# Kernel tuning notes

Measured on AMD Instinct MI355X. Metric: run time of the kernel, lower is better.

The kernel has to match this reference:

```python
import jax, jax.numpy as jnp
import numpy as np

B, S, V, F, H = 256, 512, 50000, 64, 256


def setup_inputs() -> dict:
    key = jax.random.key(0)
    ks = jax.random.split(key, 12)
    s_in = 1.0 / np.sqrt(F)
    s_hid = 1.0 / np.sqrt(H)
    return {
        "batch": jax.random.randint(ks[0], (B, S), 0, V),
        "features": jax.random.normal(ks[1], (V, F), jnp.float32),
        "W_ih0": jax.random.normal(ks[2], (H, F), jnp.float32) * s_in,
        "W_hh0": jax.random.normal(ks[3], (H, H), jnp.float32) * s_hid,
        "b_ih0": jax.random.normal(ks[4], (H,), jnp.float32) * s_hid,
        "b_hh0": jax.random.normal(ks[5], (H,), jnp.float32) * s_hid,
        "W_ih1": jax.random.normal(ks[6], (H, H), jnp.float32) * s_hid,
        "W_hh1": jax.random.normal(ks[7], (H, H), jnp.float32) * s_hid,
        "b_ih1": jax.random.normal(ks[8], (H,), jnp.float32) * s_hid,
        "b_hh1": jax.random.normal(ks[9], (H,), jnp.float32) * s_hid,
        "W_out": jax.random.normal(ks[10], (V, H), jnp.float32) * s_hid,
        "b_out": jax.random.normal(ks[11], (V,), jnp.float32) * s_hid,
    }


def _rnn_layer(x, W_ih, W_hh, b_ih, b_hh):
    # x: [B, S, Din] -> [B, S, H]; torch tanh RNN: h_t = tanh(x_t W_ih^T + b_ih + h_{t-1} W_hh^T + b_hh)
    xW = jnp.einsum('bsd,hd->bsh', x, W_ih) + (b_ih + b_hh)  # precompute input projection
    h0 = jnp.zeros((x.shape[0], W_hh.shape[0]), x.dtype)

    def step(h, xt):
        h = jnp.tanh(xt + h @ W_hh.T)
        return h, h

    _, ys = jax.lax.scan(step, h0, jnp.swapaxes(xW, 0, 1))  # scan over time
    return jnp.swapaxes(ys, 0, 1)


def reference(batch, features, W_ih0, W_hh0, b_ih0, b_hh0,
              W_ih1, W_hh1, b_ih1, b_hh1, W_out, b_out):
    # vectorized replacement of the nested per-token gather loop
    full_representation = features[batch]            # [B, S, F]
    h = _rnn_layer(full_representation, W_ih0, W_hh0, b_ih0, b_hh0)
    h = _rnn_layer(h, W_ih1, W_hh1, b_ih1, b_hh1)    # [B, S, H]
    return h[:, -1, :] @ W_out.T + b_out             # [B, V]
```

## Files before the change

### kernel.cpp

```cpp
#include <hip/hip_runtime.h>

#define B_ 256
#define S_ 512
#define V_ 50000
#define F_ 64
#define H_ 256

typedef _Float16 f16;
typedef _Float16 f16x2 __attribute__((ext_vector_type(2)));
typedef _Float16 f16x4 __attribute__((ext_vector_type(4)));
typedef _Float16 f16x8 __attribute__((ext_vector_type(8)));
typedef float f32x4 __attribute__((ext_vector_type(4)));

#define MFMA(a, b, c) __builtin_amdgcn_mfma_f32_16x16x32_f16((a), (b), (c), 0, 0, 0)

__device__ __forceinline__ f16x8 cvt8(const float4 a, const float4 b) {
    f16x8 v;
    v[0] = (f16)a.x; v[1] = (f16)a.y; v[2] = (f16)a.z; v[3] = (f16)a.w;
    v[4] = (f16)b.x; v[5] = (f16)b.y; v[6] = (f16)b.z; v[7] = (f16)b.w;
    return v;
}

__device__ __forceinline__ float fast_tanh(float x) {
    float e = __expf(2.f * x);
    float r = __builtin_amdgcn_rcpf(e + 1.f);
    return __builtin_fmaf(-2.f, r, 1.f);
}

__device__ __forceinline__ f32x4 cvt4f(const f16x4 v) {
    f32x4 r; r[0] = (float)v[0]; r[1] = (float)v[1]; r[2] = (float)v[2]; r[3] = (float)v[3];
    return r;
}
__device__ __forceinline__ f16x4 pack4(const f32x4 a, const f32x4 b) {
    f16x4 r; r[0] = (f16)(a[0] + b[0]); r[1] = (f16)(a[1] + b[1]);
    r[2] = (f16)(a[2] + b[2]); r[3] = (f16)(a[3] + b[3]);
    return r;
}
__device__ __forceinline__ f16x4 tanh4(const f32x4 a, const f32x4 b) {
    f16x4 r;
#pragma unroll
    for (int i = 0; i < 4; ++i) r[i] = (f16)fast_tanh(a[i] + b[i]);
    return r;
}

__global__ void k_init_flags(int* flags) {
    if (threadIdx.x < 128) flags[threadIdx.x] = 0;
}

__global__ __launch_bounds__(512) void k_vocab_proj(
    const float* __restrict__ feat, const float* __restrict__ Wih,
    const float* __restrict__ bi, const float* __restrict__ bh,
    f16* __restrict__ T)
{
    __shared__ char Wl[256 * 128];
    __shared__ char Xl[16 * 128];
    const int tid = threadIdx.x;
    {
        const int n = tid >> 1, k0 = (tid & 1) << 5;
#pragma unroll
        for (int k = k0; k < k0 + 32; k += 8) {
            float4 a = *(const float4*)(Wih + n * F_ + k);
            float4 b = *(const float4*)(Wih + n * F_ + k + 4);
            *(f16x8*)(Wl + n * 128 + (((k >> 3) ^ (n & 7)) << 4)) = cvt8(a, b);
        }
    }
    const int v0 = blockIdx.x * 16;
    {
        const int m = tid >> 5, k = (tid & 31) << 1;
        float2 a = *(const float2*)(feat + (v0 + m) * F_ + k);
        f16x2 v; v[0] = (f16)a.x; v[1] = (f16)a.y;
        *(f16x2*)(Xl + m * 128 + ((((k >> 3) ^ (m & 7)) << 4) | ((k & 7) << 1))) = v;
    }
    __syncthreads();
    const int lane = tid & 63, w = tid >> 6;
    const int q = lane & 15, g = lane >> 4;
#pragma unroll
    for (int nt = 0; nt < 2; ++nt) {
        const int n0 = w * 32 + nt * 16;
        const int nrow = n0 + q;
        float4 b1 = *(const float4*)(bi + n0 + g * 4);
        float4 b2 = *(const float4*)(bh + n0 + g * 4);
        f32x4 acc = {b1.x + b2.x, b1.y + b2.y, b1.z + b2.z, b1.w + b2.w};
#pragma unroll
        for (int kb = 0; kb < 2; ++kb) {
            f16x8 a = *(const f16x8*)(Wl + nrow * 128 + (((kb * 4 + g) ^ (nrow & 7)) << 4));
            f16x8 b = *(const f16x8*)(Xl + q * 128 + (((kb * 4 + g) ^ (q & 7)) << 4));
            acc = MFMA(a, b, acc);
        }
        f16x4 o; o[0] = (f16)acc[0]; o[1] = (f16)acc[1]; o[2] = (f16)acc[2]; o[3] = (f16)acc[3];
        *(f16x4*)(T + (size_t)(v0 + q) * H_ + n0 + g * 4) = o;
    }
}

__global__ __launch_bounds__(512) __attribute__((amdgpu_waves_per_eu(2, 2)))
void k_rnn_split(
    const f16* __restrict__ T, const int* __restrict__ idx,
    const float* __restrict__ Whh0, const float* __restrict__ Wih1,
    const float* __restrict__ bih1, const float* __restrict__ bhh1,
    const float* __restrict__ Whh1,
    f16* __restrict__ pbuf, int* flags, f16* __restrict__ h1out)
{
    __shared__ char hb[2][8192];
    const int wg = blockIdx.x;
    const int tid = threadIdx.x, lane = tid & 63, w = tid >> 6;
    const int q = lane & 15, g = lane >> 4;
    const int ncol = w * 32;
    const int swz = (q & 7) << 4;

    int rbase[2], wbase[2];
#pragma unroll
    for (int p2 = 0; p2 < 2; ++p2)
        rbase[p2] = q * 512 + ((p2 * 64 + g * 16) ^ swz);
#pragma unroll
    for (int tt = 0; tt < 2; ++tt)
        wbase[tt] = q * 512 + (((ncol + tt * 16 + g * 4) * 2) ^ swz);

    const int pr = (wg < 16) ? wg : wg - 16;
    const int brow = pr * 16 + q;
    const size_t prow = (size_t)brow * 512;

#define FRD(kb_, RD_) (*(const f16x8*)(hb[RD_] + rbase[(kb_) & 1] + (((kb_) >> 1) * 128)))
#define HWR(tt_, WR_) (*(f16x4*)(hb[WR_] + wbase[tt_]))
#define STEP_BAR() do { \
        asm volatile("s_waitcnt lgkmcnt(0)" ::: "memory"); \
        __builtin_amdgcn_s_barrier(); \
    } while (0)

    if (wg < 16) {
        f16x8 wA[2][8], wP[2][8];
#pragma unroll
        for (int tt = 0; tt < 2; ++tt) {
            const int n = ncol + tt * 16 + q;
#pragma unroll
            for (int kb = 0; kb < 8; ++kb) {
                const int o = n * H_ + kb * 32 + g * 8;
                wA[tt][kb] = cvt8(*(const float4*)(Whh0 + o), *(const float4*)(Whh0 + o + 4));
                wP[tt][kb] = cvt8(*(const float4*)(Wih1 + o), *(const float4*)(Wih1 + o + 4));
            }
        }
        f32x4 bs1[2];
#pragma unroll
        for (int tt = 0; tt < 2; ++tt) {
            const int n = ncol + tt * 16 + g * 4;
            float4 x = *(const float4*)(bih1 + n);
            float4 y = *(const float4*)(bhh1 + n);
            bs1[tt][0] = x.x + y.x; bs1[tt][1] = x.y + y.y;
            bs1[tt][2] = x.z + y.z; bs1[tt][3] = x.w + y.w;
        }
        {
            f32x4 z = {0.f, 0.f, 0.f, 0.f};
            *(f32x4*)(hb[1] + tid * 16) = z;
        }
        const int* idxr = idx + brow * S_;
        int* myflag = flags + wg * 8 + w;
        f16x4 xa[2], xb[2];
        {
            const size_t r0 = (size_t)idxr[0] * H_, r1 = (size_t)idxr[1] * H_;
#pragma unroll
            for (int tt = 0; tt < 2; ++tt) {
                xa[tt] = *(const f16x4*)(T + r0 + ncol + tt * 16 + g * 4);
                xb[tt] = *(const f16x4*)(T + r1 + ncol + tt * 16 + g * 4);
            }
        }
        int iA = idxr[2], iB = idxr[3];
        __syncthreads();

#define PBODY(XV, ID, RD, WR, T_) do {                                          \
                \
        f16x8 bf0 = FRD(0, RD), bf1 = FRD(1, RD), bf2 = FRD(2, RD),             \
              bf3 = FRD(3, RD), bf4 = FRD(4, RD), bf5 = FRD(5, RD),             \
              bf6 = FRD(6, RD), bf7 = FRD(7, RD);                               \
        f32x4 aL[2], aH[2];                                                     \
        _Pragma("unroll")                                                       \
        for (int tt = 0; tt < 2; ++tt) {                                        \
            aL[tt] = cvt4f(XV[tt]);                                             \
            aH[tt][0] = 0.f; aH[tt][1] = 0.f; aH[tt][2] = 0.f; aH[tt][3] = 0.f; \
        }                                                                       \
        {                 \
            const size_t rr = (size_t)ID * H_;                                  \
            _Pragma("unroll")                                                   \
            for (int tt = 0; tt < 2; ++tt)                                      \
                XV[tt] = *(const f16x4*)(T + rr + ncol + tt * 16 + g * 4);      \
            const int t4 = ((T_) + 4 < S_) ? (T_) + 4 : S_ - 1;                 \
            ID = idxr[t4];                                                      \
        }                                                                       \
                                               \
        _Pragma("unroll")                                                       \
        for (int tt = 0; tt < 2; ++tt) {                                        \
            aL[tt] = MFMA(wA[tt][0], bf0, aL[tt]);                              \
            aH[tt] = MFMA(wA[tt][4], bf4, aH[tt]);                              \
            aL[tt] = MFMA(wA[tt][1], bf1, aL[tt]);                              \
            aH[tt] = MFMA(wA[tt][5], bf5, aH[tt]);                              \
            aL[tt] = MFMA(wA[tt][2], bf2, aL[tt]);                              \
            aH[tt] = MFMA(wA[tt][6], bf6, aH[tt]);                              \
            aL[tt] = MFMA(wA[tt][3], bf3, aL[tt]);                              \
            aH[tt] = MFMA(wA[tt][7], bf7, aH[tt]);                              \
        }                                                                       \
                                  \
        _Pragma("unroll")                                                       \
        for (int tt = 0; tt < 2; ++tt) HWR(tt, WR) = tanh4(aL[tt], aH[tt]);     \
                  \
        f32x4 pL[2], pH[2];                                                     \
        _Pragma("unroll")                                                       \
        for (int tt = 0; tt < 2; ++tt) {                                        \
            pL[tt] = bs1[tt];                                                   \
            pH[tt][0] = 0.f; pH[tt][1] = 0.f; pH[tt][2] = 0.f; pH[tt][3] = 0.f; \
            pL[tt] = MFMA(wP[tt][0], bf0, pL[tt]);                              \
            pH[tt] = MFMA(wP[tt][4], bf4, pH[tt]);                              \
            pL[tt] = MFMA(wP[tt][1], bf1, pL[tt]);                              \
            pH[tt] = MFMA(wP[tt][5], bf5, pH[tt]);                              \
            pL[tt] = MFMA(wP[tt][2], bf2, pL[tt]);                              \
            pH[tt] = MFMA(wP[tt][6], bf6, pH[tt]);                              \
            pL[tt] = MFMA(wP[tt][3], bf3, pL[tt]);                              \
            pH[tt] = MFMA(wP[tt][7], bf7, pH[tt]);                              \
            *(f16x4*)(pbuf + (prow + (T_) - 1) * 256 + ncol + tt * 16 + g * 4)  \
                = pack4(pL[tt], pH[tt]);                                        \
        }                                                                       \
        if ((((T_) & 7) == 0) && lane == 0)                                     \
            __hip_atomic_store(myflag, (T_), __ATOMIC_RELEASE,                  \
                               __HIP_MEMORY_SCOPE_AGENT);                       \
        STEP_BAR();                                                             \
    } while (0)

        {
            f16x8 bf0 = FRD(0, 1), bf1 = FRD(1, 1), bf2 = FRD(2, 1), bf3 = FRD(3, 1),
                  bf4 = FRD(4, 1), bf5 = FRD(5, 1), bf6 = FRD(6, 1), bf7 = FRD(7, 1);
            f32x4 aL[2], aH[2];
#pragma unroll
            for (int tt = 0; tt < 2; ++tt) {
                aL[tt] = cvt4f(xa[tt]);
                aH[tt][0] = 0.f; aH[tt][1] = 0.f; aH[tt][2] = 0.f; aH[tt][3] = 0.f;
            }
            {
                const size_t rr = (size_t)iA * H_;
#pragma unroll
                for (int tt = 0; tt < 2; ++tt)
                    xa[tt] = *(const f16x4*)(T + rr + ncol + tt * 16 + g * 4);
                iA = idxr[4];
            }
#pragma unroll
            for (int tt = 0; tt < 2; ++tt) {
                aL[tt] = MFMA(wA[tt][0], bf0, aL[tt]);
                aH[tt] = MFMA(wA[tt][4], bf4, aH[tt]);
                aL[tt] = MFMA(wA[tt][1], bf1, aL[tt]);
                aH[tt] = MFMA(wA[tt][5], bf5, aH[tt]);
                aL[tt] = MFMA(wA[tt][2], bf2, aL[tt]);
                aH[tt] = MFMA(wA[tt][6], bf6, aH[tt]);
                aL[tt] = MFMA(wA[tt][3], bf3, aL[tt]);
                aH[tt] = MFMA(wA[tt][7], bf7, aH[tt]);
                HWR(tt, 0) = tanh4(aL[tt], aH[tt]);
            }
            STEP_BAR();
        }
        for (int t = 1; t < 511; t += 2) {
            PBODY(xb, iB, 0, 1, t);
            PBODY(xa, iA, 1, 0, t + 1);
        }
        PBODY(xb, iB, 0, 1, 511);
        {
            f16x8 bf0 = FRD(0, 1), bf1 = FRD(1, 1), bf2 = FRD(2, 1), bf3 = FRD(3, 1),
                  bf4 = FRD(4, 1), bf5 = FRD(5, 1), bf6 = FRD(6, 1), bf7 = FRD(7, 1);
            f32x4 pL[2], pH[2];
#pragma unroll
            for (int tt = 0; tt < 2; ++tt) {
                pL[tt] = bs1[tt];
                pH[tt][0] = 0.f; pH[tt][1] = 0.f; pH[tt][2] = 0.f; pH[tt][3] = 0.f;
                pL[tt] = MFMA(wP[tt][0], bf0, pL[tt]);
                pH[tt] = MFMA(wP[tt][4], bf4, pH[tt]);
                pL[tt] = MFMA(wP[tt][1], bf1, pL[tt]);
                pH[tt] = MFMA(wP[tt][5], bf5, pH[tt]);
                pL[tt] = MFMA(wP[tt][2], bf2, pL[tt]);
                pH[tt] = MFMA(wP[tt][6], bf6, pH[tt]);
                pL[tt] = MFMA(wP[tt][3], bf3, pL[tt]);
                pH[tt] = MFMA(wP[tt][7], bf7, pH[tt]);
                *(f16x4*)(pbuf + (prow + 511) * 256 + ncol + tt * 16 + g * 4)
                    = pack4(pL[tt], pH[tt]);
            }
        }
        if (lane == 0)
            __hip_atomic_store(myflag, 512, __ATOMIC_RELEASE, __HIP_MEMORY_SCOPE_AGENT);
#undef PBODY
    } else {
        f16x8 wC[2][8];
#pragma unroll
        for (int tt = 0; tt < 2; ++tt) {
            const int n = ncol + tt * 16 + q;
#pragma unroll
            for (int kb = 0; kb < 8; ++kb) {
                const int o = n * H_ + kb * 32 + g * 8;
                wC[tt][kb] = cvt8(*(const float4*)(Whh1 + o), *(const float4*)(Whh1 + o + 4));
            }
        }
        {   f32x4 z = {0.f, 0.f, 0.f, 0.f}; *(f32x4*)(hb[1] + tid * 16) = z; }
        const int* fl = flags + pr * 8;
        __syncthreads();

#define SPIN(need) do {                                                         \
        int mn;                                                                 \
        do {                                                                    \
            mn = 0x7fffffff;                                                    \
            _Pragma("unroll")                                                   \
            for (int i = 0; i < 8; ++i) {                                       \
                int v = __hip_atomic_load(fl + i, __ATOMIC_RELAXED,             \
                                          __HIP_MEMORY_SCOPE_AGENT);            \
                mn = v < mn ? v : mn;                                           \
            }                                                                   \
        } while (mn < (need));                                                  \
        __builtin_amdgcn_fence(__ATOMIC_ACQUIRE, "agent");                      \
    } while (0)

#define CBODY(PV, RD, WR, T_) do {                                              \
        f16x8 cf0 = FRD(0, RD), cf1 = FRD(1, RD), cf2 = FRD(2, RD),             \
              cf3 = FRD(3, RD), cf4 = FRD(4, RD), cf5 = FRD(5, RD),             \
              cf6 = FRD(6, RD), cf7 = FRD(7, RD);                               \
        f32x4 aL[2], aH[2];                                                     \
        _Pragma("unroll")                                                       \
        for (int tt = 0; tt < 2; ++tt) {                                        \
            aL[tt] = cvt4f(PV[tt]);                                             \
            aH[tt][0] = 0.f; aH[tt][1] = 0.f; aH[tt][2] = 0.f; aH[tt][3] = 0.f; \
        }                                                                       \
        {                                                                       \
            const int tr = ((T_) + 2 < S_) ? (T_) + 2 : S_ - 1;                 \
            _Pragma("unroll")                                                   \
            for (int tt = 0; tt < 2; ++tt)                                      \
                PV[tt] = *(const f16x4*)(pbuf + (prow + tr) * 256 + ncol + tt * 16 + g * 4); \
        }                                                                       \
        _Pragma("unroll")                                                       \
        for (int tt = 0; tt < 2; ++tt) {                                        \
            aL[tt] = MFMA(wC[tt][0], cf0, aL[tt]);                              \
            aH[tt] = MFMA(wC[tt][4], cf4, aH[tt]);                              \
            aL[tt] = MFMA(wC[tt][1], cf1, aL[tt]);                              \
            aH[tt] = MFMA(wC[tt][5], cf5, aH[tt]);                              \
            aL[tt] = MFMA(wC[tt][2], cf2, aL[tt]);                              \
            aH[tt] = MFMA(wC[tt][6], cf6, aH[tt]);                              \
            aL[tt] = MFMA(wC[tt][3], cf3, aL[tt]);                              \
            aH[tt] = MFMA(wC[tt][7], cf7, aH[tt]);                              \
        }                                                                       \
        _Pragma("unroll")                                                       \
        for (int tt = 0; tt < 2; ++tt) {                                        \
            f16x4 hv = tanh4(aL[tt], aH[tt]);                                   \
            HWR(tt, WR) = hv;                                                   \
            if ((T_) == S_ - 1)                                                 \
                *(f16x4*)(h1out + (size_t)brow * H_ + ncol + tt * 16 + g * 4) = hv; \
        }                                                                       \
        STEP_BAR();                                                             \
    } while (0)

        f16x4 pa[2], pb[2];
        SPIN(6);
#pragma unroll
        for (int tt = 0; tt < 2; ++tt) {
            pa[tt] = *(const f16x4*)(pbuf + (prow + 0) * 256 + ncol + tt * 16 + g * 4);
            pb[tt] = *(const f16x4*)(pbuf + (prow + 1) * 256 + ncol + tt * 16 + g * 4);
        }
        for (int tb = 0; tb < 512; tb += 4) {
            if (tb) {
                const int need = (tb + 6 < 512) ? tb + 6 : 512;
                SPIN(need);
            }
            CBODY(pa, 1, 0, tb);
            CBODY(pb, 0, 1, tb + 1);
            CBODY(pa, 1, 0, tb + 2);
            CBODY(pb, 0, 1, tb + 3);
        }
#undef CBODY
#undef SPIN
    }
#undef FRD
#undef HWR
#undef STEP_BAR
}

__global__ __launch_bounds__(512) void k_out(
    const f16* __restrict__ h1, const float* __restrict__ Wout,
    const float* __restrict__ bout, float* __restrict__ out)
{
    __shared__ char Hl[256 * 512];
    const int tid = threadIdx.x;
    {
        const int m = tid >> 1, half = tid & 1;
#pragma unroll
        for (int i = 0; i < 16; ++i) {
            const int blk = half * 16 + i;
            f16x8 v = *(const f16x8*)(h1 + m * H_ + blk * 8);
            *(f16x8*)(Hl + m * 512 + ((blk ^ (m & 7)) << 4)) = v;
        }
    }
    __syncthreads();
    const int lane = tid & 63, w = tid >> 6;
    const int q = lane & 15, g = lane >> 4;
    const int v0 = blockIdx.x * 80;
    f32x4 acc[5][2];
#pragma unroll
    for (int vt = 0; vt < 5; ++vt) {
        float4 bo = *(const float4*)(bout + v0 + vt * 16 + g * 4);
#pragma unroll
        for (int bt = 0; bt < 2; ++bt) {
            acc[vt][bt][0] = bo.x; acc[vt][bt][1] = bo.y;
            acc[vt][bt][2] = bo.z; acc[vt][bt][3] = bo.w;
        }
    }
#pragma unroll
    for (int kb = 0; kb < 8; ++kb) {
        f16x8 bf[2];
#pragma unroll
        for (int bt = 0; bt < 2; ++bt) {
            const int mrow = (w * 2 + bt) * 16 + q;
            bf[bt] = *(const f16x8*)(Hl + mrow * 512 + (((kb * 4 + g) ^ (mrow & 7)) << 4));
        }
#pragma unroll
        for (int vt = 0; vt < 5; ++vt) {
            const size_t vrow = v0 + vt * 16 + q;
            float4 a = *(const float4*)(Wout + vrow * H_ + kb * 32 + g * 8);
            float4 b = *(const float4*)(Wout + vrow * H_ + kb * 32 + g * 8 + 4);
            f16x8 af = cvt8(a, b);
#pragma unroll
            for (int bt = 0; bt < 2; ++bt)
                acc[vt][bt] = MFMA(af, bf[bt], acc[vt][bt]);
        }
    }
#pragma unroll
    for (int vt = 0; vt < 5; ++vt)
#pragma unroll
        for (int bt = 0; bt < 2; ++bt) {
            const int b = (w * 2 + bt) * 16 + q;
            const int v = v0 + vt * 16 + g * 4;
            float4 o = {acc[vt][bt][0], acc[vt][bt][1], acc[vt][bt][2], acc[vt][bt][3]};
            *(float4*)(out + (size_t)b * V_ + v) = o;
        }
}

extern "C" void kernel_launch(void* const* d_in, const int* in_sizes, int n_in,
                              void* d_out, int out_size, void* d_ws, size_t ws_size,
                              hipStream_t stream) {
    (void)in_sizes; (void)n_in; (void)out_size; (void)ws_size;
    const int*   batch = (const int*)  d_in[0];
    const float* feat  = (const float*)d_in[1];
    const float* Wih0  = (const float*)d_in[2];
    const float* Whh0  = (const float*)d_in[3];
    const float* bih0  = (const float*)d_in[4];
    const float* bhh0  = (const float*)d_in[5];
    const float* Wih1  = (const float*)d_in[6];
    const float* Whh1  = (const float*)d_in[7];
    const float* bih1  = (const float*)d_in[8];
    const float* bhh1  = (const float*)d_in[9];
    const float* Wout  = (const float*)d_in[10];
    const float* bout  = (const float*)d_in[11];
    float* out = (float*)d_out;

    f16* T     = (f16*)d_out;
    int* flags = (int*)((char*)d_out + 48000000);
    f16* pbuf  = (f16*)d_ws;
    f16* h1out = (f16*)((char*)d_ws + (size_t)B_ * S_ * H_ * 2);

    k_init_flags<<<dim3(1), dim3(128), 0, stream>>>(flags);
    k_vocab_proj<<<dim3(V_ / 16), dim3(512), 0, stream>>>(feat, Wih0, bih0, bhh0, T);
    k_rnn_split<<<dim3(32), dim3(512), 0, stream>>>(T, batch, Whh0, Wih1, bih1, bhh1,
                                                    Whh1, pbuf, flags, h1out);
    k_out<<<dim3(625), dim3(512), 0, stream>>>(h1out, Wout, bout, out);
}
```

Baseline: 934.5 us.

## Rebalance layer-1 input projection between producer and consumer RNN blocks with h0 ring

The RNN kernel drops from 8 to 4 waves per block, so each wave now computes 64 output columns. The layer-0 producer blocks now compute only half of the W_ih1 projection. They write the raw h0 states into a 128-step ring buffer, and the layer-1 consumer blocks compute the other half of the projection from that ring. A consumer-progress flag lets the producer throttle so it cannot overrun the ring. The aim is to balance work between the two pipeline halves and shrink the projection buffer traffic, at the cost of more registers per wave, extra back-pressure synchronisation, and ring reads on the consumer side.

```diff
diff --git a/kernel.cpp b/kernel.cpp
--- a/kernel.cpp
+++ b/kernel.cpp
@@ -40,6 +40,13 @@
     f16x4 r;
 #pragma unroll
     for (int i = 0; i < 4; ++i) r[i] = (f16)fast_tanh(a[i] + b[i]);
+    return r;
+}
+__device__ __forceinline__ f16x4 tanh4c(const f32x4 a, const f32x4 b,
+                                        const f32x4 c, const f32x4 d) {
+    f16x4 r;
+#pragma unroll
+    for (int i = 0; i < 4; ++i) r[i] = (f16)fast_tanh((a[i] + b[i]) + (c[i] + d[i]));
     return r;
 }
 
@@ -92,32 +99,34 @@
     }
 }
 
-__global__ __launch_bounds__(512) __attribute__((amdgpu_waves_per_eu(2, 2)))
-void k_rnn_split(
+__global__ __launch_bounds__(256) __attribute__((amdgpu_waves_per_eu(1, 1)))
+void k_rnn2(
     const f16* __restrict__ T, const int* __restrict__ idx,
     const float* __restrict__ Whh0, const float* __restrict__ Wih1,
     const float* __restrict__ bih1, const float* __restrict__ bhh1,
     const float* __restrict__ Whh1,
-    f16* __restrict__ pbuf, int* flags, f16* __restrict__ h1out)
+    f16* __restrict__ h0ring, f16* __restrict__ plow,
+    int* flags, f16* __restrict__ h1out)
 {
     __shared__ char hb[2][8192];
     const int wg = blockIdx.x;
     const int tid = threadIdx.x, lane = tid & 63, w = tid >> 6;
-    const int q = lane & 15, g = lane >> 4;
-    const int ncol = w * 32;
+    const int q = lane & 15, gl = lane >> 4;
+    const int ncol = w * 64;
     const int swz = (q & 7) << 4;
 
-    int rbase[2], wbase[2];
+    int rbase[2], wbase[4];
 #pragma unroll
     for (int p2 = 0; p2 < 2; ++p2)
-        rbase[p2] = q * 512 + ((p2 * 64 + g * 16) ^ swz);
-#pragma unroll
-    for (int tt = 0; tt < 2; ++tt)
-        wbase[tt] = q * 512 + (((ncol + tt * 16 + g * 4) * 2) ^ swz);
-
-    const int pr = (wg < 16) ? wg : wg - 16;
-    const int brow = pr * 16 + q;
-    const size_t prow = (size_t)brow * 512;
+        rbase[p2] = q * 512 + ((p2 * 64 + gl * 16) ^ swz);
+#pragma unroll
+    for (int tt = 0; tt < 4; ++tt)
+        wbase[tt] = q * 512 + (((ncol + tt * 16 + gl * 4) * 2) ^ swz);
+
+    int* prodf = flags;
+    int* consf = flags + 64;
+    const int gr = (wg < 16) ? wg : wg - 16;
+    const int brow = gr * 16 + q;
 
 #define FRD(kb_, RD_) (*(const f16x8*)(hb[RD_] + rbase[(kb_) & 1] + (((kb_) >> 1) * 128)))
 #define HWR(tt_, WR_) (*(f16x4*)(hb[WR_] + wbase[tt_]))
@@ -127,21 +136,22 @@
     } while (0)
 
     if (wg < 16) {
-        f16x8 wA[2][8], wP[2][8];
+        f16x8 wA[4][8], wP[2][8];
+#pragma unroll
+        for (int tt = 0; tt < 4; ++tt) {
+            const int n = ncol + tt * 16 + q;
+#pragma unroll
+            for (int kb = 0; kb < 8; ++kb) {
+                const int o = n * H_ + kb * 32 + gl * 8;
+                wA[tt][kb] = cvt8(*(const float4*)(Whh0 + o), *(const float4*)(Whh0 + o + 4));
+                if (tt < 2)
+                    wP[tt][kb] = cvt8(*(const float4*)(Wih1 + o), *(const float4*)(Wih1 + o + 4));
+            }
+        }
+        f32x4 bs1[2];
 #pragma unroll
         for (int tt = 0; tt < 2; ++tt) {
-            const int n = ncol + tt * 16 + q;
-#pragma unroll
-            for (int kb = 0; kb < 8; ++kb) {
-                const int o = n * H_ + kb * 32 + g * 8;
-                wA[tt][kb] = cvt8(*(const float4*)(Whh0 + o), *(const float4*)(Whh0 + o + 4));
-                wP[tt][kb] = cvt8(*(const float4*)(Wih1 + o), *(const float4*)(Wih1 + o + 4));
-            }
-        }
-        f32x4 bs1[2];
-#pragma unroll
-        for (int tt = 0; tt < 2; ++tt) {
-            const int n = ncol + tt * 16 + g * 4;
+            const int n = ncol + tt * 16 + gl * 4;
             float4 x = *(const float4*)(bih1 + n);
             float4 y = *(const float4*)(bhh1 + n);
             bs1[tt][0] = x.x + y.x; bs1[tt][1] = x.y + y.y;
@@ -149,44 +159,53 @@
         }
         {
             f32x4 z = {0.f, 0.f, 0.f, 0.f};
-            *(f32x4*)(hb[1] + tid * 16) = z;
+            *(f32x4*)(hb[1] + tid * 32) = z;
+            *(f32x4*)(hb[1] + tid * 32 + 16) = z;
         }
         const int* idxr = idx + brow * S_;
-        int* myflag = flags + wg * 8 + w;
-        f16x4 xa[2], xb[2];
+        int* myflag = prodf + gr * 4 + w;
+        f16x4 xa[4], xb[4];
         {
             const size_t r0 = (size_t)idxr[0] * H_, r1 = (size_t)idxr[1] * H_;
 #pragma unroll
-            for (int tt = 0; tt < 2; ++tt) {
-                xa[tt] = *(const f16x4*)(T + r0 + ncol + tt * 16 + g * 4);
-                xb[tt] = *(const f16x4*)(T + r1 + ncol + tt * 16 + g * 4);
+            for (int tt = 0; tt < 4; ++tt) {
+                xa[tt] = *(const f16x4*)(T + r0 + ncol + tt * 16 + gl * 4);
+                xb[tt] = *(const f16x4*)(T + r1 + ncol + tt * 16 + gl * 4);
             }
         }
         int iA = idxr[2], iB = idxr[3];
         __syncthreads();
 
 #define PBODY(XV, ID, RD, WR, T_) do {                                          \
-                \
+        if (((T_) & 15) == 0) {       \
+            int v_;                                                             \
+            do { v_ = __hip_atomic_load(consf + gr, __ATOMIC_RELAXED,           \
+                                        __HIP_MEMORY_SCOPE_AGENT);              \
+            } while ((T_) - v_ > 96);                                           \
+        }                                                                       \
         f16x8 bf0 = FRD(0, RD), bf1 = FRD(1, RD), bf2 = FRD(2, RD),             \
               bf3 = FRD(3, RD), bf4 = FRD(4, RD), bf5 = FRD(5, RD),             \
               bf6 = FRD(6, RD), bf7 = FRD(7, RD);                               \
-        f32x4 aL[2], aH[2];                                                     \
-        _Pragma("unroll")                                                       \
-        for (int tt = 0; tt < 2; ++tt) {                                        \
+        f32x4 aL[4], aH[4];                                                     \
+        _Pragma("unroll")                                                       \
+        for (int tt = 0; tt < 4; ++tt) {                                        \
             aL[tt] = cvt4f(XV[tt]);                                             \
             aH[tt][0] = 0.f; aH[tt][1] = 0.f; aH[tt][2] = 0.f; aH[tt][3] = 0.f; \
         }                                                                       \
-        {                 \
+         \
+        if ((((T_) & 7) == 0) && lane == 0)                                     \
+            __hip_atomic_store(myflag, (T_), __ATOMIC_RELEASE,                  \
+                               __HIP_MEMORY_SCOPE_AGENT);                       \
+        {                                                                       \
             const size_t rr = (size_t)ID * H_;                                  \
             _Pragma("unroll")                                                   \
-            for (int tt = 0; tt < 2; ++tt)                                      \
-                XV[tt] = *(const f16x4*)(T + rr + ncol + tt * 16 + g * 4);      \
+            for (int tt = 0; tt < 4; ++tt)                                      \
+                XV[tt] = *(const f16x4*)(T + rr + ncol + tt * 16 + gl * 4);     \
             const int t4 = ((T_) + 4 < S_) ? (T_) + 4 : S_ - 1;                 \
             ID = idxr[t4];                                                      \
         }                                                                       \
-                                               \
-        _Pragma("unroll")                                                       \
-        for (int tt = 0; tt < 2; ++tt) {                                        \
+        _Pragma("unroll")                                                       \
+        for (int tt = 0; tt < 4; ++tt) {                                        \
             aL[tt] = MFMA(wA[tt][0], bf0, aL[tt]);                              \
             aH[tt] = MFMA(wA[tt][4], bf4, aH[tt]);                              \
             aL[tt] = MFMA(wA[tt][1], bf1, aL[tt]);                              \
@@ -196,10 +215,6 @@
             aL[tt] = MFMA(wA[tt][3], bf3, aL[tt]);                              \
             aH[tt] = MFMA(wA[tt][7], bf7, aH[tt]);                              \
         }                                                                       \
-                                  \
-        _Pragma("unroll")                                                       \
-        for (int tt = 0; tt < 2; ++tt) HWR(tt, WR) = tanh4(aL[tt], aH[tt]);     \
-                  \
         f32x4 pL[2], pH[2];                                                     \
         _Pragma("unroll")                                                       \
         for (int tt = 0; tt < 2; ++tt) {                                        \
@@ -213,33 +228,39 @@
             pH[tt] = MFMA(wP[tt][6], bf6, pH[tt]);                              \
             pL[tt] = MFMA(wP[tt][3], bf3, pL[tt]);                              \
             pH[tt] = MFMA(wP[tt][7], bf7, pH[tt]);                              \
-            *(f16x4*)(pbuf + (prow + (T_) - 1) * 256 + ncol + tt * 16 + g * 4)  \
-                = pack4(pL[tt], pH[tt]);                                        \
-        }                                                                       \
-        if ((((T_) & 7) == 0) && lane == 0)                                     \
-            __hip_atomic_store(myflag, (T_), __ATOMIC_RELEASE,                  \
-                               __HIP_MEMORY_SCOPE_AGENT);                       \
+        }                                                                       \
+        const size_t rs = ((size_t)(gr * 128 + ((T_) & 127)) * 16 + q) * 256;   \
+        _Pragma("unroll")                                                       \
+        for (int tt = 0; tt < 4; ++tt) {                                        \
+            f16x4 hv = tanh4(aL[tt], aH[tt]);                                   \
+            HWR(tt, WR) = hv;                                                   \
+            *(f16x4*)(h0ring + rs + ncol + tt * 16 + gl * 4) = hv;              \
+        }                                                                       \
+        _Pragma("unroll")                                                       \
+        for (int tt = 0; tt < 2; ++tt)                                          \
+            *(f16x4*)(plow + ((size_t)brow * 512 + (T_) - 1) * 128              \
+                      + 32 * w + tt * 16 + gl * 4) = pack4(pL[tt], pH[tt]);     \
         STEP_BAR();                                                             \
     } while (0)
 
         {
             f16x8 bf0 = FRD(0, 1), bf1 = FRD(1, 1), bf2 = FRD(2, 1), bf3 = FRD(3, 1),
                   bf4 = FRD(4, 1), bf5 = FRD(5, 1), bf6 = FRD(6, 1), bf7 = FRD(7, 1);
-            f32x4 aL[2], aH[2];
-#pragma unroll
-            for (int tt = 0; tt < 2; ++tt) {
+            f32x4 aL[4], aH[4];
+#pragma unroll
+            for (int tt = 0; tt < 4; ++tt) {
                 aL[tt] = cvt4f(xa[tt]);
                 aH[tt][0] = 0.f; aH[tt][1] = 0.f; aH[tt][2] = 0.f; aH[tt][3] = 0.f;
             }
             {
                 const size_t rr = (size_t)iA * H_;
 #pragma unroll
-                for (int tt = 0; tt < 2; ++tt)
-                    xa[tt] = *(const f16x4*)(T + rr + ncol + tt * 16 + g * 4);
+                for (int tt = 0; tt < 4; ++tt)
+                    xa[tt] = *(const f16x4*)(T + rr + ncol + tt * 16 + gl * 4);
                 iA = idxr[4];
             }
 #pragma unroll
-            for (int tt = 0; tt < 2; ++tt) {
+            for (int tt = 0; tt < 4; ++tt) {
                 aL[tt] = MFMA(wA[tt][0], bf0, aL[tt]);
                 aH[tt] = MFMA(wA[tt][4], bf4, aH[tt]);
                 aL[tt] = MFMA(wA[tt][1], bf1, aL[tt]);
@@ -248,7 +269,13 @@
                 aH[tt] = MFMA(wA[tt][6], bf6, aH[tt]);
                 aL[tt] = MFMA(wA[tt][3], bf3, aL[tt]);
                 aH[tt] = MFMA(wA[tt][7], bf7, aH[tt]);
-                HWR(tt, 0) = tanh4(aL[tt], aH[tt]);
+            }
+            const size_t rs = ((size_t)(gr * 128) * 16 + q) * 256;
+#pragma unroll
+            for (int tt = 0; tt < 4; ++tt) {
+                f16x4 hv = tanh4(aL[tt], aH[tt]);
+                HWR(tt, 0) = hv;
+                *(f16x4*)(h0ring + rs + ncol + tt * 16 + gl * 4) = hv;
             }
             STEP_BAR();
         }
@@ -273,39 +300,53 @@
                 pH[tt] = MFMA(wP[tt][6], bf6, pH[tt]);
                 pL[tt] = MFMA(wP[tt][3], bf3, pL[tt]);
                 pH[tt] = MFMA(wP[tt][7], bf7, pH[tt]);
-                *(f16x4*)(pbuf + (prow + 511) * 256 + ncol + tt * 16 + g * 4)
-                    = pack4(pL[tt], pH[tt]);
+                *(f16x4*)(plow + ((size_t)brow * 512 + 511) * 128
+                          + 32 * w + tt * 16 + gl * 4) = pack4(pL[tt], pH[tt]);
             }
         }
         if (lane == 0)
             __hip_atomic_store(myflag, 512, __ATOMIC_RELEASE, __HIP_MEMORY_SCOPE_AGENT);
 #undef PBODY
     } else {
-        f16x8 wC[2][8];
+        f16x8 wC[4][8], wPh[2][8];
+#pragma unroll
+        for (int tt = 0; tt < 4; ++tt) {
+            const int n = ncol + tt * 16 + q;
+#pragma unroll
+            for (int kb = 0; kb < 8; ++kb) {
+                const int o = n * H_ + kb * 32 + gl * 8;
+                wC[tt][kb] = cvt8(*(const float4*)(Whh1 + o), *(const float4*)(Whh1 + o + 4));
+                if (tt >= 2)
+                    wPh[tt - 2][kb] = cvt8(*(const float4*)(Wih1 + o), *(const float4*)(Wih1 + o + 4));
+            }
+        }
+        f32x4 bsh[2];
 #pragma unroll
         for (int tt = 0; tt < 2; ++tt) {
-            const int n = ncol + tt * 16 + q;
-#pragma unroll
-            for (int kb = 0; kb < 8; ++kb) {
-                const int o = n * H_ + kb * 32 + g * 8;
-                wC[tt][kb] = cvt8(*(const float4*)(Whh1 + o), *(const float4*)(Whh1 + o + 4));
-            }
-        }
-        {   f32x4 z = {0.f, 0.f, 0.f, 0.f}; *(f32x4*)(hb[1] + tid * 16) = z; }
-        const int* fl = flags + pr * 8;
+            const int n = ncol + (tt + 2) * 16 + gl * 4;
+            float4 x = *(const float4*)(bih1 + n);
+            float4 y = *(const float4*)(bhh1 + n);
+            bsh[tt][0] = x.x + y.x; bsh[tt][1] = x.y + y.y;
+            bsh[tt][2] = x.z + y.z; bsh[tt][3] = x.w + y.w;
+        }
+        {
+            f32x4 z = {0.f, 0.f, 0.f, 0.f};
+            *(f32x4*)(hb[1] + tid * 32) = z;
+            *(f32x4*)(hb[1] + tid * 32 + 16) = z;
+        }
         __syncthreads();
 
 #define SPIN(need) do {                                                         \
-        int mn;                                                                 \
+        int mn_;                                                                \
         do {                                                                    \
-            mn = 0x7fffffff;                                                    \
+            mn_ = 0x7fffffff;                                                   \
             _Pragma("unroll")                                                   \
-            for (int i = 0; i < 8; ++i) {                                       \
-                int v = __hip_atomic_load(fl + i, __ATOMIC_RELAXED,             \
-                                          __HIP_MEMORY_SCOPE_AGENT);            \
-                mn = v < mn ? v : mn;                                           \
+            for (int i_ = 0; i_ < 4; ++i_) {                                    \
+                int v_ = __hip_atomic_load(prodf + gr * 4 + i_, __ATOMIC_RELAXED, \
+                                           __HIP_MEMORY_SCOPE_AGENT);           \
+                mn_ = v_ < mn_ ? v_ : mn_;                                      \
             }                                                                   \
-        } while (mn < (need));                                                  \
+        } while (mn_ < (need));                                                 \
         __builtin_amdgcn_fence(__ATOMIC_ACQUIRE, "agent");                      \
     } while (0)
 
@@ -313,55 +354,90 @@
         f16x8 cf0 = FRD(0, RD), cf1 = FRD(1, RD), cf2 = FRD(2, RD),             \
               cf3 = FRD(3, RD), cf4 = FRD(4, RD), cf5 = FRD(5, RD),             \
               cf6 = FRD(6, RD), cf7 = FRD(7, RD);                               \
-        f32x4 aL[2], aH[2];                                                     \
-        _Pragma("unroll")                                                       \
-        for (int tt = 0; tt < 2; ++tt) {                                        \
-            aL[tt] = cvt4f(PV[tt]);                                             \
-            aH[tt][0] = 0.f; aH[tt][1] = 0.f; aH[tt][2] = 0.f; aH[tt][3] = 0.f; \
-        }                                                                       \
-        {                                                                       \
+        f32x4 cL[4], cH[4];                                                     \
+        cL[0] = cvt4f(PV[0]); cL[1] = cvt4f(PV[1]);                             \
+        cL[2] = bsh[0]; cL[3] = bsh[1];                                         \
+        _Pragma("unroll")                                                       \
+        for (int tt = 0; tt < 4; ++tt) {                                        \
+            cH[tt][0] = 0.f; cH[tt][1] = 0.f; cH[tt][2] = 0.f; cH[tt][3] = 0.f; \
+        }                                                                       \
+        f32x4 pL[2], pH[2];                                                     \
+        _Pragma("unroll")                                                       \
+        for (int i = 0; i < 2; ++i) {                                           \
+            pL[i][0] = 0.f; pL[i][1] = 0.f; pL[i][2] = 0.f; pL[i][3] = 0.f;     \
+            pH[i] = pL[i];                                                      \
+            pL[i] = MFMA(wPh[i][0], HF[0], pL[i]);                              \
+            pH[i] = MFMA(wPh[i][4], HF[4], pH[i]);                              \
+            pL[i] = MFMA(wPh[i][1], HF[1], pL[i]);                              \
+            pH[i] = MFMA(wPh[i][5], HF[5], pH[i]);                              \
+            pL[i] = MFMA(wPh[i][2], HF[2], pL[i]);                              \
+            pH[i] = MFMA(wPh[i][6], HF[6], pH[i]);                              \
+            pL[i] = MFMA(wPh[i][3], HF[3], pL[i]);                              \
+            pH[i] = MFMA(wPh[i][7], HF[7], pH[i]);                              \
+        }                                                                       \
+        {                      \
+            const int s1 = ((T_) + 1 < S_) ? (T_) + 1 : S_ - 1;                 \
+            const size_t rbb = ((size_t)(gr * 128 + (s1 & 127)) * 16 + q) * 256 + gl * 8; \
+            _Pragma("unroll")                                                   \
+            for (int j = 0; j < 8; ++j)                                         \
+                HF[j] = *(const f16x8*)(h0ring + rbb + j * 32);                 \
+        }                                                                       \
+        {                                          \
             const int tr = ((T_) + 2 < S_) ? (T_) + 2 : S_ - 1;                 \
             _Pragma("unroll")                                                   \
-            for (int tt = 0; tt < 2; ++tt)                                      \
-                PV[tt] = *(const f16x4*)(pbuf + (prow + tr) * 256 + ncol + tt * 16 + g * 4); \
-        }                                                                       \
-        _Pragma("unroll")                                                       \
-        for (int tt = 0; tt < 2; ++tt) {                                        \
-            aL[tt] = MFMA(wC[tt][0], cf0, aL[tt]);                              \
-            aH[tt] = MFMA(wC[tt][4], cf4, aH[tt]);                              \
-            aL[tt] = MFMA(wC[tt][1], cf1, aL[tt]);                              \
-            aH[tt] = MFMA(wC[tt][5], cf5, aH[tt]);                              \
-            aL[tt] = MFMA(wC[tt][2], cf2, aL[tt]);                              \
-            aH[tt] = MFMA(wC[tt][6], cf6, aH[tt]);                              \
-            aL[tt] = MFMA(wC[tt][3], cf3, aL[tt]);                              \
-            aH[tt] = MFMA(wC[tt][7], cf7, aH[tt]);                              \
-        }                                                                       \
-        _Pragma("unroll")                                                       \
-        for (int tt = 0; tt < 2; ++tt) {                                        \
-            f16x4 hv = tanh4(aL[tt], aH[tt]);                                   \
-            HWR(tt, WR) = hv;                                                   \
-            if ((T_) == S_ - 1)                                                 \
-                *(f16x4*)(h1out + (size_t)brow * H_ + ncol + tt * 16 + g * 4) = hv; \
+            for (int i = 0; i < 2; ++i)                                         \
+                PV[i] = *(const f16x4*)(plow + ((size_t)brow * 512 + tr) * 128  \
+                                        + 32 * w + i * 16 + gl * 4);            \
+        }                                                                       \
+        _Pragma("unroll")                                                       \
+        for (int tt = 0; tt < 4; ++tt) {                                        \
+            cL[tt] = MFMA(wC[tt][0], cf0, cL[tt]);                              \
+            cH[tt] = MFMA(wC[tt][4], cf4, cH[tt]);                              \
+            cL[tt] = MFMA(wC[tt][1], cf1, cL[tt]);                              \
+            cH[tt] = MFMA(wC[tt][5], cf5, cH[tt]);                              \
+            cL[tt] = MFMA(wC[tt][2], cf2, cL[tt]);                              \
+            cH[tt] = MFMA(wC[tt][6], cf6, cH[tt]);                              \
+            cL[tt] = MFMA(wC[tt][3], cf3, cL[tt]);                              \
+            cH[tt] = MFMA(wC[tt][7], cf7, cH[tt]);                              \
+        }                                                                       \
+        f16x4 hv0 = tanh4(cL[0], cH[0]);                                        \
+        f16x4 hv1 = tanh4(cL[1], cH[1]);                                        \
+        f16x4 hv2 = tanh4c(cL[2], cH[2], pL[0], pH[0]);                         \
+        f16x4 hv3 = tanh4c(cL[3], cH[3], pL[1], pH[1]);                         \
+        HWR(0, WR) = hv0; HWR(1, WR) = hv1; HWR(2, WR) = hv2; HWR(3, WR) = hv3; \
+        if ((T_) == S_ - 1) {                                                   \
+            *(f16x4*)(h1out + (size_t)brow * H_ + ncol + 0 * 16 + gl * 4) = hv0; \
+            *(f16x4*)(h1out + (size_t)brow * H_ + ncol + 1 * 16 + gl * 4) = hv1; \
+            *(f16x4*)(h1out + (size_t)brow * H_ + ncol + 2 * 16 + gl * 4) = hv2; \
+            *(f16x4*)(h1out + (size_t)brow * H_ + ncol + 3 * 16 + gl * 4) = hv3; \
         }                                                                       \
         STEP_BAR();                                                             \
     } while (0)
 
         f16x4 pa[2], pb[2];
-        SPIN(6);
-#pragma unroll
-        for (int tt = 0; tt < 2; ++tt) {
-            pa[tt] = *(const f16x4*)(pbuf + (prow + 0) * 256 + ncol + tt * 16 + g * 4);
-            pb[tt] = *(const f16x4*)(pbuf + (prow + 1) * 256 + ncol + tt * 16 + g * 4);
-        }
-        for (int tb = 0; tb < 512; tb += 4) {
-            if (tb) {
-                const int need = (tb + 6 < 512) ? tb + 6 : 512;
+        f16x8 HF[8];
+        SPIN(14);
+        {
+#pragma unroll
+            for (int i = 0; i < 2; ++i) {
+                pa[i] = *(const f16x4*)(plow + ((size_t)brow * 512 + 0) * 128 + 32 * w + i * 16 + gl * 4);
+                pb[i] = *(const f16x4*)(plow + ((size_t)brow * 512 + 1) * 128 + 32 * w + i * 16 + gl * 4);
+            }
+            const size_t rbb = ((size_t)(gr * 128) * 16 + q) * 256 + gl * 8;
+#pragma unroll
+            for (int j = 0; j < 8; ++j)
+                HF[j] = *(const f16x8*)(h0ring + rbb + j * 32);
+        }
+        for (int t = 0; t < 512; t += 2) {
+            if (t && ((t & 7) == 0)) {
+                if (tid == 0)
+                    __hip_atomic_store(consf + gr, t, __ATOMIC_RELEASE,
+                                       __HIP_MEMORY_SCOPE_AGENT);
+                const int need = (t + 14 < 512) ? t + 14 : 512;
                 SPIN(need);
             }
-            CBODY(pa, 1, 0, tb);
-            CBODY(pb, 0, 1, tb + 1);
-            CBODY(pa, 1, 0, tb + 2);
-            CBODY(pb, 0, 1, tb + 3);
+            CBODY(pa, 1, 0, t);
+            CBODY(pb, 0, 1, t + 1);
         }
 #undef CBODY
 #undef SPIN
@@ -448,14 +524,15 @@
     const float* bout  = (const float*)d_in[11];
     float* out = (float*)d_out;
 
-    f16* T     = (f16*)d_out;
-    int* flags = (int*)((char*)d_out + 48000000);
-    f16* pbuf  = (f16*)d_ws;
-    f16* h1out = (f16*)((char*)d_ws + (size_t)B_ * S_ * H_ * 2);
+    f16* T      = (f16*)d_out;
+    f16* h0ring = (f16*)((char*)d_out + 27000000);
+    int* flags  = (int*)((char*)d_out + 48000000);
+    f16* plow   = (f16*)d_ws;
+    f16* h1out  = (f16*)((char*)d_ws + (size_t)B_ * S_ * 128 * 2);
 
     k_init_flags<<<dim3(1), dim3(128), 0, stream>>>(flags);
     k_vocab_proj<<<dim3(V_ / 16), dim3(512), 0, stream>>>(feat, Wih0, bih0, bhh0, T);
-    k_rnn_split<<<dim3(32), dim3(512), 0, stream>>>(T, batch, Whh0, Wih1, bih1, bhh1,
-                                                    Whh1, pbuf, flags, h1out);
+    k_rnn2<<<dim3(32), dim3(256), 0, stream>>>(T, batch, Whh0, Wih1, bih1, bhh1,
+                                               Whh1, h0ring, plow, flags, h1out);
     k_out<<<dim3(625), dim3(512), 0, stream>>>(h1out, Wout, bout, out);
 }
```

Measured after the change: 955.1 us. +2.2%, slower.
